# Kernel tuning notes

Hardware: AMD Instinct MI355X
Metric: run time of the kernel (lower is better)

## Reference

```python
import jax, jax.numpy as jnp
import numpy as np

H = W = 32          # gussin() is hard-coded to width=32 in BASE
C = 512             # BASE inner_nc; down conv is 1024->512
V = 1.5             # gaussian sigma


def _gaussian_weights():
    # Vectorized equivalent of gussin(1.5): g[p, x, y] for p = i*W + k,
    # g = exp(-((x-i)^2+(y-k)^2)/(2 v^2)) / (2 pi v^2), normalized per p.
    idx = np.arange(H, dtype=np.float64)
    d1 = (idx[:, None] - idx[None, :]) ** 2            # (i, x)
    d2 = d1[:, None, :, None] + d1[None, :, None, :]    # (i, k, x, y)
    g = np.exp(-d2 / (2.0 * V * V)) / (2.0 * np.pi * V * V)
    g = g.reshape(H * W, H, W)
    g = g / g.sum(axis=(1, 2), keepdims=True)
    return jnp.asarray(g, dtype=jnp.float32)


def _instance_norm(x, eps=1e-5):
    # InstanceNorm2d(affine=False): per-(b,c) mean/biased-var over (h,w)
    mu = x.mean(axis=(2, 3), keepdims=True)
    var = jnp.mean((x - mu) ** 2, axis=(2, 3), keepdims=True)
    return (x - mu) / jnp.sqrt(var + eps)


def _patches3(fm):
    # fm: (C, H+2, W+2) zero-padded map -> 3x3 patches: (H*W, C, 3, 3)
    p = jnp.stack([fm[:, di:di + H, dj:dj + W]
                   for di in range(3) for dj in range(3)], axis=-1)  # (C,H,W,9)
    return p.transpose(1, 2, 0, 3).reshape(H * W, C, 3, 3)


def setup_inputs() -> dict:
    key = jax.random.key(0)
    ks = jax.random.split(key, 4)
    x = jax.random.normal(ks[0], (1, C, H, W), jnp.float32)
    w_se1 = jax.random.normal(ks[1], (C // 16, C), jnp.float32) * 0.05   # SE squeeze fc
    w_se2 = jax.random.normal(ks[2], (C, C // 16), jnp.float32) * 0.05   # SE excite fc
    w_down = jax.random.normal(ks[3], (C, 2 * C, 1, 1), jnp.float32) * 0.05  # 1x1 conv 1024->512
    return {"x": x, "w_se1": w_se1, "w_se2": w_se2, "w_down": w_down}


def reference(x, w_se1, w_se2, w_down):
    gus = _gaussian_weights()                                # (HW, H, W), constant
    # --- SELayer(512, 16) ---
    s = x.mean(axis=(2, 3))                                  # (1, C) global avg pool
    s = jax.nn.relu(s @ w_se1.T)                             # (1, C/16)
    s = jax.nn.sigmoid(s @ w_se2.T)                          # (1, C)
    out32 = x * s[:, :, None, None]                          # (1, C, H, W)
    # --- gaussian-weighted pooling (einsum instead of (HW,C,H,W) broadcast) ---
    gus_out = jnp.einsum('pxy,cxy->pc', gus, out32[0])       # (HW, C)
    gus_out = gus_out.reshape(1, C, H, W)                    # raw reshape, as in torch .view
    # --- patch-based contextual self-attention (CSA) ---
    sig = jax.nn.sigmoid(out32)                              # (1, C, H, W)
    sig_pad = jnp.pad(sig[0], ((0, 0), (1, 1), (1, 1)))
    raw_pad = jnp.pad(out32[0], ((0, 0), (1, 1), (1, 1)))
    p_sig = _patches3(sig_pad)                               # (HW, C, 3, 3)
    p_raw = _patches3(raw_pad)                               # (HW, C, 3, 3)
    center = sig[0].transpose(1, 2, 0).reshape(H * W, C, 1, 1)  # center sigmoid vec per loc
    score = jnp.mean(center * p_sig, axis=1)                 # (HW, 3, 3)
    attn = jax.nn.softmax(score.reshape(H * W, 9), axis=1).reshape(H * W, 1, 3, 3)
    out_csa = jnp.sum(attn * p_raw, axis=(2, 3))             # (HW, C)
    out_csa = out_csa.reshape(1, C, H, W)                    # raw reshape, as in torch .view
    # --- concat + 1x1 conv down + InstanceNorm + LeakyReLU(0.2) ---
    cat = jnp.concatenate([gus_out, out_csa], axis=1)        # (1, 2C, H, W)
    y = jnp.einsum('bihw,oi->bohw', cat, w_down[:, :, 0, 0])
    y = _instance_norm(y)
    return jnp.where(y >= 0, y, 0.2 * y)
```

## Files before the change

### kernel.cpp

```cpp
#include <hip/hip_runtime.h>


typedef short short8 __attribute__((ext_vector_type(8)));
typedef short short4v __attribute__((ext_vector_type(4)));
typedef float floatx4 __attribute__((ext_vector_type(4)));

__device__ __forceinline__ unsigned short f2bf(float x) {
  union { float f; unsigned u; } v; v.f = x;
  unsigned u = v.u;
  u = (u + 0x7fffu + ((u >> 16) & 1u)) >> 16;
  return (unsigned short)u;
}

__device__ __forceinline__ float block_reduce_256(float v, float* sm4) {
  #pragma unroll
  for (int off = 32; off >= 1; off >>= 1) v += __shfl_down(v, off);
  __syncthreads();
  if ((threadIdx.x & 63) == 0) sm4[threadIdx.x >> 6] = v;
  __syncthreads();
  return sm4[0] + sm4[1] + sm4[2] + sm4[3];
}

__global__ void k_mean_gn(const float* __restrict__ x, float* __restrict__ smean,
                          float* __restrict__ gn, const float* __restrict__ wdn,
                          unsigned short* __restrict__ Abf) {
  if (blockIdx.x > 512) {
    int base = (blockIdx.x - 513) * 2048 + threadIdx.x * 8;
    float4 a = *(const float4*)&wdn[base];
    float4 b = *(const float4*)&wdn[base + 4];
    short8 s;
    s[0] = (short)f2bf(a.x); s[1] = (short)f2bf(a.y); s[2] = (short)f2bf(a.z); s[3] = (short)f2bf(a.w);
    s[4] = (short)f2bf(b.x); s[5] = (short)f2bf(b.y); s[6] = (short)f2bf(b.z); s[7] = (short)f2bf(b.w);
    *(short8*)&Abf[base] = s;
    return;
  }
  if (blockIdx.x == 512) {
    int tid = threadIdx.x;
    int a = tid >> 3;
    int b0 = (tid & 7) * 4;
    float e[4];
    float s = 0.0f;
    #pragma unroll
    for (int q = 0; q < 4; q++) {
      float d = (float)(a - (b0 + q));
      e[q] = __expf(d * d * (-1.0f / 4.5f));
      s += e[q];
    }
    s += __shfl_xor(s, 1, 8);
    s += __shfl_xor(s, 2, 8);
    s += __shfl_xor(s, 4, 8);
    float inv = 1.0f / s;
    #pragma unroll
    for (int q = 0; q < 4; q++) gn[a * 32 + b0 + q] = e[q] * inv;
    return;
  }
  __shared__ float sm4[4];
  int c = blockIdx.x;
  const float* row = x + c * 1024;
  float s = 0.0f;
  for (int i = threadIdx.x; i < 1024; i += 256) s += row[i];
  float t = block_reduce_256(s, sm4);
  if (threadIdx.x == 0) smean[c] = t * (1.0f / 1024.0f);
}

__global__ void k_apply(const float* __restrict__ x, const float* __restrict__ smean,
                        const float* __restrict__ w1, const float* __restrict__ w2,
                        float* __restrict__ out32T, float* __restrict__ sigT,
                        float* __restrict__ V) {
  __shared__ float sm[512];
  __shared__ float s1[32];
  __shared__ float sc[32];
  __shared__ float tile[32][33];
  int tid = threadIdx.x;
  for (int i = tid; i < 512; i += 256) sm[i] = smean[i];
  __syncthreads();
  int j = tid >> 3, l8 = tid & 7;
  float a = 0.0f;
  for (int cc = l8; cc < 512; cc += 8) a += sm[cc] * w1[j * 512 + cc];
  a += __shfl_down(a, 4, 8);
  a += __shfl_down(a, 2, 8);
  a += __shfl_down(a, 1, 8);
  if (l8 == 0) s1[j] = fmaxf(a, 0.0f);
  __syncthreads();
  int c0 = blockIdx.y * 32, hw0 = blockIdx.x * 32;
  if (tid < 32) {
    float b = 0.0f;
    #pragma unroll
    for (int jj = 0; jj < 32; jj++) b += s1[jj] * w2[(c0 + tid) * 32 + jj];
    sc[tid] = 1.0f / (1.0f + __expf(-b));
  }
  __syncthreads();
  int tx = tid & 31, ty = tid >> 5;
  #pragma unroll
  for (int r = 0; r < 4; r++) {
    int c = ty + 8 * r;
    float v = x[(c0 + c) * 1024 + hw0 + tx] * sc[c];
    tile[c][tx] = v;
  }
  __syncthreads();
  #pragma unroll
  for (int r = 0; r < 4; r++) {
    int hw = hw0 + ty + 8 * r;
    float v = tile[tx][ty + 8 * r];
    out32T[hw * 512 + c0 + tx] = v;
    sigT[hw * 512 + c0 + tx] = 1.0f / (1.0f + __expf(-v));
    int hwsw = ((hw & 31) << 5) | (hw >> 5);
    V[hwsw * 512 + c0 + tx] = v;
  }
}

__global__ void k_g1csa(const float* __restrict__ V, const float* __restrict__ gn,
                        const float* __restrict__ sigT, const float* __restrict__ out32T,
                        float* __restrict__ T1, unsigned short* __restrict__ catT) {
  if (blockIdx.x < 512) {
    __shared__ float g[1024];
    int tid = threadIdx.x;
    for (int i = tid; i < 1024; i += 256) g[i] = gn[i];
    __syncthreads();
    int t = blockIdx.x * 256 + tid;
    int c = t & 511;
    int xk = t >> 9;
    int xx = xk & 31, kg = xk >> 5;
    const float* vp = V + xx * 512 + c;
    const float* g0 = g + kg * 4 * 32;
    float s0 = 0, s1 = 0, s2 = 0, s3 = 0;
    #pragma unroll 8
    for (int y = 0; y < 32; y++) {
      float vv = vp[y * 16384];
      s0 += g0[y] * vv;
      s1 += g0[32 + y] * vv;
      s2 += g0[64 + y] * vv;
      s3 += g0[96 + y] * vv;
    }
    int ko = kg * 4 * 32 + xx;
    T1[ko * 512 + c] = s0;
    T1[(ko + 32) * 512 + c] = s1;
    T1[(ko + 64) * 512 + c] = s2;
    T1[(ko + 96) * 512 + c] = s3;
  } else {
    int wv = threadIdx.x >> 6;
    int lane = threadIdx.x & 63;
    int p = (blockIdx.x - 512) * 4 + wv;
    int h = p >> 5, w = p & 31;
    int c0 = lane * 8;
    float4 ce0 = *(const float4*)&sigT[p * 512 + c0];
    float4 ce1 = *(const float4*)&sigT[p * 512 + c0 + 4];
    int qoff[9];
    float s[9];
    #pragma unroll
    for (int dd = 0; dd < 9; dd++) {
      int hh = h + dd / 3 - 1, ww = w + (dd % 3) - 1;
      bool v = (hh >= 0) && (hh < 32) && (ww >= 0) && (ww < 32);
      qoff[dd] = v ? (hh * 32 + ww) * 512 : -1;
      float a = 0.0f;
      if (v) {
        float4 n0 = *(const float4*)&sigT[qoff[dd] + c0];
        float4 n1 = *(const float4*)&sigT[qoff[dd] + c0 + 4];
        a = ce0.x * n0.x + ce0.y * n0.y + ce0.z * n0.z + ce0.w * n0.w
          + ce1.x * n1.x + ce1.y * n1.y + ce1.z * n1.z + ce1.w * n1.w;
      }
      #pragma unroll
      for (int off = 32; off >= 1; off >>= 1) a += __shfl_xor(a, off);
      s[dd] = a;
    }
    float mx = -1e30f;
    #pragma unroll
    for (int dd = 0; dd < 9; dd++) { s[dd] *= (1.0f / 512.0f); mx = fmaxf(mx, s[dd]); }
    float tot = 0.0f;
    #pragma unroll
    for (int dd = 0; dd < 9; dd++) { s[dd] = __expf(s[dd] - mx); tot += s[dd]; }
    float inv = 1.0f / tot;
    float o[8] = {0, 0, 0, 0, 0, 0, 0, 0};
    #pragma unroll
    for (int dd = 0; dd < 9; dd++) {
      if (qoff[dd] >= 0) {
        float att = s[dd] * inv;
        float4 r0 = *(const float4*)&out32T[qoff[dd] + c0];
        float4 r1 = *(const float4*)&out32T[qoff[dd] + c0 + 4];
        o[0] += att * r0.x; o[1] += att * r0.y; o[2] += att * r0.z; o[3] += att * r0.w;
        o[4] += att * r1.x; o[5] += att * r1.y; o[6] += att * r1.z; o[7] += att * r1.w;
      }
    }
    int kcol = 512 + (p >> 1);
    int nbase = (p & 1) * 512 + c0;
    #pragma unroll
    for (int q = 0; q < 8; q++) catT[(nbase + q) * 1024 + kcol] = f2bf(o[q]);
  }
}

__global__ void k_g2(const float* __restrict__ T1, const float* __restrict__ gn,
                     unsigned short* __restrict__ catT) {
  __shared__ float g[1024];
  int tid = threadIdx.x;
  for (int i = tid; i < 1024; i += 256) g[i] = gn[i];
  __syncthreads();
  int t = blockIdx.x * 256 + tid;
  int c = t & 511;
  int rest = t >> 9;
  int i = rest >> 3;
  int sub = rest & 7;
  int par = sub & 1, kq = sub >> 1;
  const float* tp = T1 + c;
  const float* gi = g + i * 32;
  float s0 = 0, s1 = 0, s2 = 0, s3 = 0;
  int kb = kq * 8 + par;
  #pragma unroll 8
  for (int xx = 0; xx < 32; xx++) {
    float gv = gi[xx];
    s0 += gv * tp[((kb + 0) * 32 + xx) * 512];
    s1 += gv * tp[((kb + 2) * 32 + xx) * 512];
    s2 += gv * tp[((kb + 4) * 32 + xx) * 512];
    s3 += gv * tp[((kb + 6) * 32 + xx) * 512];
  }
  short4v o;
  o[0] = (short)f2bf(s0); o[1] = (short)f2bf(s1); o[2] = (short)f2bf(s2); o[3] = (short)f2bf(s3);
  *(short4v*)&catT[(par * 512 + c) * 1024 + i * 16 + kq * 4] = o;
}

__global__ void k_gemm(const unsigned short* __restrict__ Abf,
                       const unsigned short* __restrict__ Bbf,
                       float* __restrict__ yp) {
  int wv = threadIdx.x >> 6, lane = threadIdx.x & 63;
  int w0 = blockIdx.x;
  int m = w0 >> 4;
  int n0 = (w0 & 15) * 64;
  int nn = n0 + (wv & 1) * 32;
  int kz = wv >> 1;
  int l16 = lane & 15, quad = lane >> 4;
  const short8* ap  = (const short8*)(Abf + (m * 16 + l16) * 1024 + kz * 512 + quad * 8);
  const short8* bp0 = (const short8*)(Bbf + (nn + l16) * 1024 + kz * 512 + quad * 8);
  const short8* bp1 = (const short8*)(Bbf + (nn + 16 + l16) * 1024 + kz * 512 + quad * 8);
  floatx4 acc0 = {0.f, 0.f, 0.f, 0.f}, acc1 = {0.f, 0.f, 0.f, 0.f};
  #pragma unroll 4
  for (int kk = 0; kk < 16; kk++) {
    short8 a  = ap[kk * 4];
    short8 b0 = bp0[kk * 4];
    short8 b1 = bp1[kk * 4];
    acc0 = __builtin_amdgcn_mfma_f32_16x16x32_bf16(a, b0, acc0, 0, 0, 0);
    acc1 = __builtin_amdgcn_mfma_f32_16x16x32_bf16(a, b1, acc1, 0, 0, 0);
  }
  float* yo = yp + kz * 524288 + (m * 16 + quad * 4) * 1024 + l16;
  #pragma unroll
  for (int r = 0; r < 4; r++) {
    yo[r * 1024 + nn] = acc0[r];
    yo[r * 1024 + nn + 16] = acc1[r];
  }
}

__global__ void k_inorm(const float* __restrict__ yp, float* __restrict__ out) {
  __shared__ float sm4[4];
  __shared__ float vrow[1024];
  int o = blockIdx.x;
  const float* r0 = yp + o * 1024;
  float s = 0.0f, q = 0.0f;
  for (int i = threadIdx.x; i < 1024; i += 256) {
    float v = r0[i] + r0[i + 524288];
    vrow[i] = v;
    s += v; q += v * v;
  }
  float ts = block_reduce_256(s, sm4);
  float tq = block_reduce_256(q, sm4);
  float mean = ts * (1.0f / 1024.0f);
  float var = tq * (1.0f / 1024.0f) - mean * mean;
  float inv = rsqrtf(var + 1e-5f);
  for (int i = threadIdx.x; i < 1024; i += 256) {
    float v = (vrow[i] - mean) * inv;
    out[o * 1024 + i] = v >= 0.0f ? v : 0.2f * v;
  }
}

extern "C" void kernel_launch(void* const* d_in, const int* in_sizes, int n_in,
                              void* d_out, int out_size, void* d_ws, size_t ws_size,
                              hipStream_t stream) {
  const float* x      = (const float*)d_in[0];
  const float* w_se1  = (const float*)d_in[1];
  const float* w_se2  = (const float*)d_in[2];
  const float* w_down = (const float*)d_in[3];
  float* out = (float*)d_out;

  float* ws = (float*)d_ws;
  float* gn     = ws;
  float* smean  = ws + 1024;
  float* out32T = ws + 2048;
  float* sigT   = out32T + 524288;
  float* V      = sigT + 524288;
  float* T1     = V + 524288;
  unsigned short* catT = (unsigned short*)(T1 + 524288);
  unsigned short* Abf  = (unsigned short*)(T1 + 1048576);
  float* yp     = T1 + 1310720;

  k_mean_gn<<<769, 256, 0, stream>>>(x, smean, gn, w_down, Abf);
  k_apply<<<dim3(32, 16), 256, 0, stream>>>(x, smean, w_se1, w_se2, out32T, sigT, V);
  k_g1csa<<<768, 256, 0, stream>>>(V, gn, sigT, out32T, T1, catT);
  k_g2<<<512, 256, 0, stream>>>(T1, gn, catT);
  k_gemm<<<512, 256, 0, stream>>>(Abf, catT, yp);
  k_inorm<<<512, 256, 0, stream>>>(yp, out);
}
```

Measured before the change: 111.7 us.

## Fuse six kernels into one persistent kernel with atomic grid barriers

Replaces the six-kernel launch sequence with a single persistent kernel of 512 blocks. The stages are separated by software grid barriers built on atomic counters, which are reset by a memset before launch. The Gaussian table is now computed per block straight into shared memory instead of staged through global memory, and the CSA work is moved into two waves of the same blocks that run the first Gaussian pass. The aim is to remove launch gaps and inter-kernel drain; the cost is barrier spin overhead and a deadlock risk if not all 512 blocks are co-resident.

Result: slower. 357.9 us (+220.5%).

```diff
diff --git a/kernel.cpp b/kernel.cpp
--- a/kernel.cpp
+++ b/kernel.cpp
@@ -4,6 +4,8 @@
 typedef short short8 __attribute__((ext_vector_type(8)));
 typedef short short4v __attribute__((ext_vector_type(4)));
 typedef float floatx4 __attribute__((ext_vector_type(4)));
+
+#define NBLK 512
 
 __device__ __forceinline__ unsigned short f2bf(float x) {
   union { float f; unsigned u; } v; v.f = x;
@@ -21,251 +23,251 @@
   return sm4[0] + sm4[1] + sm4[2] + sm4[3];
 }
 
-__global__ void k_mean_gn(const float* __restrict__ x, float* __restrict__ smean,
-                          float* __restrict__ gn, const float* __restrict__ wdn,
-                          unsigned short* __restrict__ Abf) {
-  if (blockIdx.x > 512) {
-    int base = (blockIdx.x - 513) * 2048 + threadIdx.x * 8;
-    float4 a = *(const float4*)&wdn[base];
-    float4 b = *(const float4*)&wdn[base + 4];
-    short8 s;
-    s[0] = (short)f2bf(a.x); s[1] = (short)f2bf(a.y); s[2] = (short)f2bf(a.z); s[3] = (short)f2bf(a.w);
-    s[4] = (short)f2bf(b.x); s[5] = (short)f2bf(b.y); s[6] = (short)f2bf(b.z); s[7] = (short)f2bf(b.w);
-    *(short8*)&Abf[base] = s;
-    return;
-  }
-  if (blockIdx.x == 512) {
-    int tid = threadIdx.x;
-    int a = tid >> 3;
-    int b0 = (tid & 7) * 4;
-    float e[4];
-    float s = 0.0f;
-    #pragma unroll
-    for (int q = 0; q < 4; q++) {
-      float d = (float)(a - (b0 + q));
-      e[q] = __expf(d * d * (-1.0f / 4.5f));
-      s += e[q];
-    }
-    s += __shfl_xor(s, 1, 8);
-    s += __shfl_xor(s, 2, 8);
-    s += __shfl_xor(s, 4, 8);
-    float inv = 1.0f / s;
-    #pragma unroll
-    for (int q = 0; q < 4; q++) gn[a * 32 + b0 + q] = e[q] * inv;
-    return;
-  }
+__device__ __forceinline__ void gridbar(int* cnt, int ph) {
+  __syncthreads();
+  if (threadIdx.x == 0) {
+    __threadfence();
+    __hip_atomic_fetch_add(&cnt[ph], 1, __ATOMIC_RELAXED, __HIP_MEMORY_SCOPE_AGENT);
+    int it = 0;
+    while (__hip_atomic_load(&cnt[ph], __ATOMIC_RELAXED, __HIP_MEMORY_SCOPE_AGENT) < NBLK) {
+      __builtin_amdgcn_s_sleep(2);
+      if (++it > (1 << 24)) break;
+    }
+    __threadfence();
+  }
+  __syncthreads();
+}
+
+__global__ __launch_bounds__(256, 2) void k_fused(
+    const float* __restrict__ x, const float* __restrict__ w1,
+    const float* __restrict__ w2, const float* __restrict__ wdn,
+    int* __restrict__ cnt, float* __restrict__ smean,
+    float* __restrict__ out32T, float* __restrict__ sigT,
+    float* __restrict__ V, float* __restrict__ T1,
+    unsigned short* __restrict__ catT, unsigned short* __restrict__ Abf,
+    float* __restrict__ yp, float* __restrict__ out) {
   __shared__ float sm4[4];
-  int c = blockIdx.x;
-  const float* row = x + c * 1024;
-  float s = 0.0f;
-  for (int i = threadIdx.x; i < 1024; i += 256) s += row[i];
-  float t = block_reduce_256(s, sm4);
-  if (threadIdx.x == 0) smean[c] = t * (1.0f / 1024.0f);
-}
-
-__global__ void k_apply(const float* __restrict__ x, const float* __restrict__ smean,
-                        const float* __restrict__ w1, const float* __restrict__ w2,
-                        float* __restrict__ out32T, float* __restrict__ sigT,
-                        float* __restrict__ V) {
   __shared__ float sm[512];
   __shared__ float s1[32];
   __shared__ float sc[32];
   __shared__ float tile[32][33];
-  int tid = threadIdx.x;
-  for (int i = tid; i < 512; i += 256) sm[i] = smean[i];
-  __syncthreads();
-  int j = tid >> 3, l8 = tid & 7;
-  float a = 0.0f;
-  for (int cc = l8; cc < 512; cc += 8) a += sm[cc] * w1[j * 512 + cc];
-  a += __shfl_down(a, 4, 8);
-  a += __shfl_down(a, 2, 8);
-  a += __shfl_down(a, 1, 8);
-  if (l8 == 0) s1[j] = fmaxf(a, 0.0f);
-  __syncthreads();
-  int c0 = blockIdx.y * 32, hw0 = blockIdx.x * 32;
-  if (tid < 32) {
-    float b = 0.0f;
-    #pragma unroll
-    for (int jj = 0; jj < 32; jj++) b += s1[jj] * w2[(c0 + tid) * 32 + jj];
-    sc[tid] = 1.0f / (1.0f + __expf(-b));
-  }
-  __syncthreads();
-  int tx = tid & 31, ty = tid >> 5;
-  #pragma unroll
-  for (int r = 0; r < 4; r++) {
-    int c = ty + 8 * r;
-    float v = x[(c0 + c) * 1024 + hw0 + tx] * sc[c];
-    tile[c][tx] = v;
-  }
-  __syncthreads();
-  #pragma unroll
-  for (int r = 0; r < 4; r++) {
-    int hw = hw0 + ty + 8 * r;
-    float v = tile[tx][ty + 8 * r];
-    out32T[hw * 512 + c0 + tx] = v;
-    sigT[hw * 512 + c0 + tx] = 1.0f / (1.0f + __expf(-v));
-    int hwsw = ((hw & 31) << 5) | (hw >> 5);
-    V[hwsw * 512 + c0 + tx] = v;
-  }
-}
-
-__global__ void k_g1csa(const float* __restrict__ V, const float* __restrict__ gn,
-                        const float* __restrict__ sigT, const float* __restrict__ out32T,
-                        float* __restrict__ T1, unsigned short* __restrict__ catT) {
-  if (blockIdx.x < 512) {
-    __shared__ float g[1024];
-    int tid = threadIdx.x;
-    for (int i = tid; i < 1024; i += 256) g[i] = gn[i];
-    __syncthreads();
-    int t = blockIdx.x * 256 + tid;
+  __shared__ float g[1024];
+  __shared__ float vrow[1024];
+
+  const int tid = threadIdx.x;
+  const int b = blockIdx.x;
+
+  {
+    const float* row = x + b * 1024;
+    float s = 0.0f;
+    #pragma unroll
+    for (int i = tid; i < 1024; i += 256) s += row[i];
+    float t = block_reduce_256(s, sm4);
+    if (tid == 0) smean[b] = t * (1.0f / 1024.0f);
+    int base = b * 1024 + tid * 4;
+    float4 a4 = *(const float4*)&wdn[base];
+    short4v s4;
+    s4[0] = (short)f2bf(a4.x); s4[1] = (short)f2bf(a4.y);
+    s4[2] = (short)f2bf(a4.z); s4[3] = (short)f2bf(a4.w);
+    *(short4v*)&Abf[base] = s4;
+    int ga = tid >> 3, gb0 = (tid & 7) * 4;
+    float e[4]; float gs = 0.0f;
+    #pragma unroll
+    for (int q = 0; q < 4; q++) {
+      float d = (float)(ga - (gb0 + q));
+      e[q] = __expf(d * d * (-1.0f / 4.5f));
+      gs += e[q];
+    }
+    gs += __shfl_xor(gs, 1, 8);
+    gs += __shfl_xor(gs, 2, 8);
+    gs += __shfl_xor(gs, 4, 8);
+    float ginv = 1.0f / gs;
+    #pragma unroll
+    for (int q = 0; q < 4; q++) g[ga * 32 + gb0 + q] = e[q] * ginv;
+  }
+  gridbar(cnt, 0);
+
+  {
+    for (int i = tid; i < 512; i += 256) sm[i] = smean[i];
+    __syncthreads();
+    int j = tid >> 3, l8 = tid & 7;
+    float a = 0.0f;
+    for (int cc = l8; cc < 512; cc += 8) a += sm[cc] * w1[j * 512 + cc];
+    a += __shfl_down(a, 4, 8);
+    a += __shfl_down(a, 2, 8);
+    a += __shfl_down(a, 1, 8);
+    if (l8 == 0) s1[j] = fmaxf(a, 0.0f);
+    __syncthreads();
+    int c0 = (b & 15) * 32, hw0 = (b >> 4) * 32;
+    if (tid < 32) {
+      float bb = 0.0f;
+      #pragma unroll
+      for (int jj = 0; jj < 32; jj++) bb += s1[jj] * w2[(c0 + tid) * 32 + jj];
+      sc[tid] = 1.0f / (1.0f + __expf(-bb));
+    }
+    __syncthreads();
+    int tx = tid & 31, ty = tid >> 5;
+    #pragma unroll
+    for (int r = 0; r < 4; r++) {
+      int c = ty + 8 * r;
+      tile[c][tx] = x[(c0 + c) * 1024 + hw0 + tx] * sc[c];
+    }
+    __syncthreads();
+    #pragma unroll
+    for (int r = 0; r < 4; r++) {
+      int hw = hw0 + ty + 8 * r;
+      float v = tile[tx][ty + 8 * r];
+      out32T[hw * 512 + c0 + tx] = v;
+      sigT[hw * 512 + c0 + tx] = 1.0f / (1.0f + __expf(-v));
+      int hwsw = ((hw & 31) << 5) | (hw >> 5);
+      V[hwsw * 512 + c0 + tx] = v;
+    }
+  }
+  gridbar(cnt, 1);
+
+  {
+    int t = b * 256 + tid;
     int c = t & 511;
     int xk = t >> 9;
     int xx = xk & 31, kg = xk >> 5;
     const float* vp = V + xx * 512 + c;
-    const float* g0 = g + kg * 4 * 32;
-    float s0 = 0, s1 = 0, s2 = 0, s3 = 0;
+    const float* g0 = g + kg * 128;
+    float s0 = 0, s1v = 0, s2 = 0, s3 = 0;
     #pragma unroll 8
     for (int y = 0; y < 32; y++) {
       float vv = vp[y * 16384];
       s0 += g0[y] * vv;
-      s1 += g0[32 + y] * vv;
+      s1v += g0[32 + y] * vv;
       s2 += g0[64 + y] * vv;
       s3 += g0[96 + y] * vv;
     }
-    int ko = kg * 4 * 32 + xx;
+    int ko = kg * 128 + xx;
     T1[ko * 512 + c] = s0;
-    T1[(ko + 32) * 512 + c] = s1;
+    T1[(ko + 32) * 512 + c] = s1v;
     T1[(ko + 64) * 512 + c] = s2;
     T1[(ko + 96) * 512 + c] = s3;
-  } else {
-    int wv = threadIdx.x >> 6;
-    int lane = threadIdx.x & 63;
-    int p = (blockIdx.x - 512) * 4 + wv;
-    int h = p >> 5, w = p & 31;
-    int c0 = lane * 8;
-    float4 ce0 = *(const float4*)&sigT[p * 512 + c0];
-    float4 ce1 = *(const float4*)&sigT[p * 512 + c0 + 4];
-    int qoff[9];
-    float s[9];
-    #pragma unroll
-    for (int dd = 0; dd < 9; dd++) {
-      int hh = h + dd / 3 - 1, ww = w + (dd % 3) - 1;
-      bool v = (hh >= 0) && (hh < 32) && (ww >= 0) && (ww < 32);
-      qoff[dd] = v ? (hh * 32 + ww) * 512 : -1;
-      float a = 0.0f;
-      if (v) {
-        float4 n0 = *(const float4*)&sigT[qoff[dd] + c0];
-        float4 n1 = *(const float4*)&sigT[qoff[dd] + c0 + 4];
-        a = ce0.x * n0.x + ce0.y * n0.y + ce0.z * n0.z + ce0.w * n0.w
-          + ce1.x * n1.x + ce1.y * n1.y + ce1.z * n1.z + ce1.w * n1.w;
+
+    int wv = tid >> 6, lane = tid & 63;
+    if (wv < 2) {
+      int p = b * 2 + wv;
+      int h = p >> 5, w = p & 31;
+      int c0 = lane * 8;
+      float4 ce0 = *(const float4*)&sigT[p * 512 + c0];
+      float4 ce1 = *(const float4*)&sigT[p * 512 + c0 + 4];
+      int qoff[9];
+      float s[9];
+      #pragma unroll
+      for (int dd = 0; dd < 9; dd++) {
+        int hh = h + dd / 3 - 1, ww = w + (dd % 3) - 1;
+        bool v = (hh >= 0) && (hh < 32) && (ww >= 0) && (ww < 32);
+        qoff[dd] = v ? (hh * 32 + ww) * 512 : -1;
+        float a = 0.0f;
+        if (v) {
+          float4 n0 = *(const float4*)&sigT[qoff[dd] + c0];
+          float4 n1 = *(const float4*)&sigT[qoff[dd] + c0 + 4];
+          a = ce0.x * n0.x + ce0.y * n0.y + ce0.z * n0.z + ce0.w * n0.w
+            + ce1.x * n1.x + ce1.y * n1.y + ce1.z * n1.z + ce1.w * n1.w;
+        }
+        #pragma unroll
+        for (int off = 32; off >= 1; off >>= 1) a += __shfl_xor(a, off);
+        s[dd] = a;
       }
-      #pragma unroll
-      for (int off = 32; off >= 1; off >>= 1) a += __shfl_xor(a, off);
-      s[dd] = a;
-    }
-    float mx = -1e30f;
-    #pragma unroll
-    for (int dd = 0; dd < 9; dd++) { s[dd] *= (1.0f / 512.0f); mx = fmaxf(mx, s[dd]); }
-    float tot = 0.0f;
-    #pragma unroll
-    for (int dd = 0; dd < 9; dd++) { s[dd] = __expf(s[dd] - mx); tot += s[dd]; }
-    float inv = 1.0f / tot;
-    float o[8] = {0, 0, 0, 0, 0, 0, 0, 0};
-    #pragma unroll
-    for (int dd = 0; dd < 9; dd++) {
-      if (qoff[dd] >= 0) {
-        float att = s[dd] * inv;
-        float4 r0 = *(const float4*)&out32T[qoff[dd] + c0];
-        float4 r1 = *(const float4*)&out32T[qoff[dd] + c0 + 4];
-        o[0] += att * r0.x; o[1] += att * r0.y; o[2] += att * r0.z; o[3] += att * r0.w;
-        o[4] += att * r1.x; o[5] += att * r1.y; o[6] += att * r1.z; o[7] += att * r1.w;
+      float mx = -1e30f;
+      #pragma unroll
+      for (int dd = 0; dd < 9; dd++) { s[dd] *= (1.0f / 512.0f); mx = fmaxf(mx, s[dd]); }
+      float tot = 0.0f;
+      #pragma unroll
+      for (int dd = 0; dd < 9; dd++) { s[dd] = __expf(s[dd] - mx); tot += s[dd]; }
+      float inv = 1.0f / tot;
+      float o[8] = {0, 0, 0, 0, 0, 0, 0, 0};
+      #pragma unroll
+      for (int dd = 0; dd < 9; dd++) {
+        if (qoff[dd] >= 0) {
+          float att = s[dd] * inv;
+          float4 r0 = *(const float4*)&out32T[qoff[dd] + c0];
+          float4 r1 = *(const float4*)&out32T[qoff[dd] + c0 + 4];
+          o[0] += att * r0.x; o[1] += att * r0.y; o[2] += att * r0.z; o[3] += att * r0.w;
+          o[4] += att * r1.x; o[5] += att * r1.y; o[6] += att * r1.z; o[7] += att * r1.w;
+        }
       }
-    }
-    int kcol = 512 + (p >> 1);
-    int nbase = (p & 1) * 512 + c0;
-    #pragma unroll
-    for (int q = 0; q < 8; q++) catT[(nbase + q) * 1024 + kcol] = f2bf(o[q]);
-  }
-}
-
-__global__ void k_g2(const float* __restrict__ T1, const float* __restrict__ gn,
-                     unsigned short* __restrict__ catT) {
-  __shared__ float g[1024];
-  int tid = threadIdx.x;
-  for (int i = tid; i < 1024; i += 256) g[i] = gn[i];
-  __syncthreads();
-  int t = blockIdx.x * 256 + tid;
-  int c = t & 511;
-  int rest = t >> 9;
-  int i = rest >> 3;
-  int sub = rest & 7;
-  int par = sub & 1, kq = sub >> 1;
-  const float* tp = T1 + c;
-  const float* gi = g + i * 32;
-  float s0 = 0, s1 = 0, s2 = 0, s3 = 0;
-  int kb = kq * 8 + par;
-  #pragma unroll 8
-  for (int xx = 0; xx < 32; xx++) {
-    float gv = gi[xx];
-    s0 += gv * tp[((kb + 0) * 32 + xx) * 512];
-    s1 += gv * tp[((kb + 2) * 32 + xx) * 512];
-    s2 += gv * tp[((kb + 4) * 32 + xx) * 512];
-    s3 += gv * tp[((kb + 6) * 32 + xx) * 512];
-  }
-  short4v o;
-  o[0] = (short)f2bf(s0); o[1] = (short)f2bf(s1); o[2] = (short)f2bf(s2); o[3] = (short)f2bf(s3);
-  *(short4v*)&catT[(par * 512 + c) * 1024 + i * 16 + kq * 4] = o;
-}
-
-__global__ void k_gemm(const unsigned short* __restrict__ Abf,
-                       const unsigned short* __restrict__ Bbf,
-                       float* __restrict__ yp) {
-  int wv = threadIdx.x >> 6, lane = threadIdx.x & 63;
-  int w0 = blockIdx.x;
-  int m = w0 >> 4;
-  int n0 = (w0 & 15) * 64;
-  int nn = n0 + (wv & 1) * 32;
-  int kz = wv >> 1;
-  int l16 = lane & 15, quad = lane >> 4;
-  const short8* ap  = (const short8*)(Abf + (m * 16 + l16) * 1024 + kz * 512 + quad * 8);
-  const short8* bp0 = (const short8*)(Bbf + (nn + l16) * 1024 + kz * 512 + quad * 8);
-  const short8* bp1 = (const short8*)(Bbf + (nn + 16 + l16) * 1024 + kz * 512 + quad * 8);
-  floatx4 acc0 = {0.f, 0.f, 0.f, 0.f}, acc1 = {0.f, 0.f, 0.f, 0.f};
-  #pragma unroll 4
-  for (int kk = 0; kk < 16; kk++) {
-    short8 a  = ap[kk * 4];
-    short8 b0 = bp0[kk * 4];
-    short8 b1 = bp1[kk * 4];
-    acc0 = __builtin_amdgcn_mfma_f32_16x16x32_bf16(a, b0, acc0, 0, 0, 0);
-    acc1 = __builtin_amdgcn_mfma_f32_16x16x32_bf16(a, b1, acc1, 0, 0, 0);
-  }
-  float* yo = yp + kz * 524288 + (m * 16 + quad * 4) * 1024 + l16;
-  #pragma unroll
-  for (int r = 0; r < 4; r++) {
-    yo[r * 1024 + nn] = acc0[r];
-    yo[r * 1024 + nn + 16] = acc1[r];
-  }
-}
-
-__global__ void k_inorm(const float* __restrict__ yp, float* __restrict__ out) {
-  __shared__ float sm4[4];
-  __shared__ float vrow[1024];
-  int o = blockIdx.x;
-  const float* r0 = yp + o * 1024;
-  float s = 0.0f, q = 0.0f;
-  for (int i = threadIdx.x; i < 1024; i += 256) {
-    float v = r0[i] + r0[i + 524288];
-    vrow[i] = v;
-    s += v; q += v * v;
-  }
-  float ts = block_reduce_256(s, sm4);
-  float tq = block_reduce_256(q, sm4);
-  float mean = ts * (1.0f / 1024.0f);
-  float var = tq * (1.0f / 1024.0f) - mean * mean;
-  float inv = rsqrtf(var + 1e-5f);
-  for (int i = threadIdx.x; i < 1024; i += 256) {
-    float v = (vrow[i] - mean) * inv;
-    out[o * 1024 + i] = v >= 0.0f ? v : 0.2f * v;
+      int kcol = 512 + (p >> 1);
+      int nbase = (p & 1) * 512 + c0;
+      #pragma unroll
+      for (int q = 0; q < 8; q++) catT[(nbase + q) * 1024 + kcol] = f2bf(o[q]);
+    }
+  }
+  gridbar(cnt, 2);
+
+  {
+    int t = b * 256 + tid;
+    int c = t & 511;
+    int rest = t >> 9;
+    int i = rest >> 3;
+    int sub = rest & 7;
+    int par = sub & 1, kq = sub >> 1;
+    int kb = kq * 8 + par;
+    const float* tp = T1 + c;
+    const float* gi = g + i * 32;
+    float s0 = 0, s1v = 0, s2 = 0, s3 = 0;
+    #pragma unroll 8
+    for (int xx = 0; xx < 32; xx++) {
+      float gv = gi[xx];
+      s0 += gv * tp[((kb + 0) * 32 + xx) * 512];
+      s1v += gv * tp[((kb + 2) * 32 + xx) * 512];
+      s2 += gv * tp[((kb + 4) * 32 + xx) * 512];
+      s3 += gv * tp[((kb + 6) * 32 + xx) * 512];
+    }
+    short4v o;
+    o[0] = (short)f2bf(s0); o[1] = (short)f2bf(s1v);
+    o[2] = (short)f2bf(s2); o[3] = (short)f2bf(s3);
+    *(short4v*)&catT[(par * 512 + c) * 1024 + i * 16 + kq * 4] = o;
+  }
+  gridbar(cnt, 3);
+
+  {
+    int wv = tid >> 6, lane = tid & 63;
+    int m = b >> 4;
+    int nn = (b & 15) * 64 + (wv & 1) * 32;
+    int kz = wv >> 1;
+    int l16 = lane & 15, quad = lane >> 4;
+    const short8* ap  = (const short8*)(Abf + (m * 16 + l16) * 1024 + kz * 512 + quad * 8);
+    const short8* bp0 = (const short8*)(catT + (nn + l16) * 1024 + kz * 512 + quad * 8);
+    const short8* bp1 = (const short8*)(catT + (nn + 16 + l16) * 1024 + kz * 512 + quad * 8);
+    floatx4 acc0 = {0.f, 0.f, 0.f, 0.f}, acc1 = {0.f, 0.f, 0.f, 0.f};
+    #pragma unroll 4
+    for (int kk = 0; kk < 16; kk++) {
+      short8 a  = ap[kk * 4];
+      short8 b0 = bp0[kk * 4];
+      short8 b1 = bp1[kk * 4];
+      acc0 = __builtin_amdgcn_mfma_f32_16x16x32_bf16(a, b0, acc0, 0, 0, 0);
+      acc1 = __builtin_amdgcn_mfma_f32_16x16x32_bf16(a, b1, acc1, 0, 0, 0);
+    }
+    float* yo = yp + kz * 524288 + (m * 16 + quad * 4) * 1024 + l16;
+    #pragma unroll
+    for (int r = 0; r < 4; r++) {
+      yo[r * 1024 + nn] = acc0[r];
+      yo[r * 1024 + nn + 16] = acc1[r];
+    }
+  }
+  gridbar(cnt, 4);
+
+  {
+    const float* r0 = yp + b * 1024;
+    float s = 0.0f, q = 0.0f;
+    for (int i = tid; i < 1024; i += 256) {
+      float v = r0[i] + r0[i + 524288];
+      vrow[i] = v;
+      s += v; q += v * v;
+    }
+    float ts = block_reduce_256(s, sm4);
+    float tq = block_reduce_256(q, sm4);
+    float mean = ts * (1.0f / 1024.0f);
+    float var = tq * (1.0f / 1024.0f) - mean * mean;
+    float inv = rsqrtf(var + 1e-5f);
+    for (int i = tid; i < 1024; i += 256) {
+      float v = (vrow[i] - mean) * inv;
+      out[b * 1024 + i] = v >= 0.0f ? v : 0.2f * v;
+    }
   }
 }
 
@@ -279,20 +281,17 @@
   float* out = (float*)d_out;
 
   float* ws = (float*)d_ws;
-  float* gn     = ws;
+  int*   cnt    = (int*)ws;
   float* smean  = ws + 1024;
   float* out32T = ws + 2048;
-  float* sigT   = out32T + 524288;
-  float* V      = sigT + 524288;
-  float* T1     = V + 524288;
-  unsigned short* catT = (unsigned short*)(T1 + 524288);
-  unsigned short* Abf  = (unsigned short*)(T1 + 1048576);
-  float* yp     = T1 + 1310720;
-
-  k_mean_gn<<<769, 256, 0, stream>>>(x, smean, gn, w_down, Abf);
-  k_apply<<<dim3(32, 16), 256, 0, stream>>>(x, smean, w_se1, w_se2, out32T, sigT, V);
-  k_g1csa<<<768, 256, 0, stream>>>(V, gn, sigT, out32T, T1, catT);
-  k_g2<<<512, 256, 0, stream>>>(T1, gn, catT);
-  k_gemm<<<512, 256, 0, stream>>>(Abf, catT, yp);
-  k_inorm<<<512, 256, 0, stream>>>(yp, out);
-}
+  float* sigT   = ws + 526336;
+  float* V      = ws + 1050624;
+  float* T1     = ws + 1574912;
+  unsigned short* catT = (unsigned short*)(ws + 2099200);
+  unsigned short* Abf  = (unsigned short*)(ws + 2623488);
+  float* yp     = ws + 2885632;
+
+  hipMemsetAsync(cnt, 0, 64, stream);
+  k_fused<<<NBLK, 256, 0, stream>>>(x, w_se1, w_se2, w_down, cnt, smean,
+                                    out32T, sigT, V, T1, catT, Abf, yp, out);
+}
```

## Fuse separable gaussian passes per channel in LDS and use 32x32 MFMA GEMM

Applied to the files above, without the earlier changes.

The two separable gaussian-filter passes are merged into one block per channel that keeps the 32x32 map and the intermediate in shared memory. This removes the T1 global round trip, the swizzled V buffer and one kernel launch. Gaussian weights are now computed inside each block instead of by a separate block. The GEMM switches to 32x32x16 bf16 MFMA and reduces the split-K partial sums in LDS, so the instance-norm kernel no longer adds two partial buffers. The price is an extra plain-layout out32 write in k_apply and redundant per-block gaussian computation.

Result: faster. 102.8 us (-7.9%).

```diff
diff --git a/kernel.cpp b/kernel.cpp
--- a/kernel.cpp
+++ b/kernel.cpp
@@ -4,6 +4,7 @@
 typedef short short8 __attribute__((ext_vector_type(8)));
 typedef short short4v __attribute__((ext_vector_type(4)));
 typedef float floatx4 __attribute__((ext_vector_type(4)));
+typedef float floatx16 __attribute__((ext_vector_type(16)));
 
 __device__ __forceinline__ unsigned short f2bf(float x) {
   union { float f; unsigned u; } v; v.f = x;
@@ -21,11 +22,27 @@
   return sm4[0] + sm4[1] + sm4[2] + sm4[3];
 }
 
-__global__ void k_mean_gn(const float* __restrict__ x, float* __restrict__ smean,
-                          float* __restrict__ gn, const float* __restrict__ wdn,
-                          unsigned short* __restrict__ Abf) {
-  if (blockIdx.x > 512) {
-    int base = (blockIdx.x - 513) * 2048 + threadIdx.x * 8;
+__device__ __forceinline__ void gauss_lds(float* g, int tid) {
+  int ga = tid >> 3, gb0 = (tid & 7) * 4;
+  float e[4]; float gs = 0.0f;
+  #pragma unroll
+  for (int q = 0; q < 4; q++) {
+    float d = (float)(ga - (gb0 + q));
+    e[q] = __expf(d * d * (-1.0f / 4.5f));
+    gs += e[q];
+  }
+  gs += __shfl_xor(gs, 1, 8);
+  gs += __shfl_xor(gs, 2, 8);
+  gs += __shfl_xor(gs, 4, 8);
+  float ginv = 1.0f / gs;
+  #pragma unroll
+  for (int q = 0; q < 4; q++) g[ga * 32 + gb0 + q] = e[q] * ginv;
+}
+
+__global__ void k_mean_cvt(const float* __restrict__ x, float* __restrict__ smean,
+                           const float* __restrict__ wdn, unsigned short* __restrict__ Abf) {
+  if (blockIdx.x >= 512) {
+    int base = (blockIdx.x - 512) * 2048 + threadIdx.x * 8;
     float4 a = *(const float4*)&wdn[base];
     float4 b = *(const float4*)&wdn[base + 4];
     short8 s;
@@ -34,26 +51,6 @@
     *(short8*)&Abf[base] = s;
     return;
   }
-  if (blockIdx.x == 512) {
-    int tid = threadIdx.x;
-    int a = tid >> 3;
-    int b0 = (tid & 7) * 4;
-    float e[4];
-    float s = 0.0f;
-    #pragma unroll
-    for (int q = 0; q < 4; q++) {
-      float d = (float)(a - (b0 + q));
-      e[q] = __expf(d * d * (-1.0f / 4.5f));
-      s += e[q];
-    }
-    s += __shfl_xor(s, 1, 8);
-    s += __shfl_xor(s, 2, 8);
-    s += __shfl_xor(s, 4, 8);
-    float inv = 1.0f / s;
-    #pragma unroll
-    for (int q = 0; q < 4; q++) gn[a * 32 + b0 + q] = e[q] * inv;
-    return;
-  }
   __shared__ float sm4[4];
   int c = blockIdx.x;
   const float* row = x + c * 1024;
@@ -65,8 +62,8 @@
 
 __global__ void k_apply(const float* __restrict__ x, const float* __restrict__ smean,
                         const float* __restrict__ w1, const float* __restrict__ w2,
-                        float* __restrict__ out32T, float* __restrict__ sigT,
-                        float* __restrict__ V) {
+                        float* __restrict__ out32, float* __restrict__ out32T,
+                        float* __restrict__ sigT) {
   __shared__ float sm[512];
   __shared__ float s1[32];
   __shared__ float sc[32];
@@ -84,10 +81,10 @@
   __syncthreads();
   int c0 = blockIdx.y * 32, hw0 = blockIdx.x * 32;
   if (tid < 32) {
-    float b = 0.0f;
-    #pragma unroll
-    for (int jj = 0; jj < 32; jj++) b += s1[jj] * w2[(c0 + tid) * 32 + jj];
-    sc[tid] = 1.0f / (1.0f + __expf(-b));
+    float bb = 0.0f;
+    #pragma unroll
+    for (int jj = 0; jj < 32; jj++) bb += s1[jj] * w2[(c0 + tid) * 32 + jj];
+    sc[tid] = 1.0f / (1.0f + __expf(-bb));
   }
   __syncthreads();
   int tx = tid & 31, ty = tid >> 5;
@@ -95,6 +92,7 @@
   for (int r = 0; r < 4; r++) {
     int c = ty + 8 * r;
     float v = x[(c0 + c) * 1024 + hw0 + tx] * sc[c];
+    out32[(c0 + c) * 1024 + hw0 + tx] = v;
     tile[c][tx] = v;
   }
   __syncthreads();
@@ -104,39 +102,61 @@
     float v = tile[tx][ty + 8 * r];
     out32T[hw * 512 + c0 + tx] = v;
     sigT[hw * 512 + c0 + tx] = 1.0f / (1.0f + __expf(-v));
-    int hwsw = ((hw & 31) << 5) | (hw >> 5);
-    V[hwsw * 512 + c0 + tx] = v;
-  }
-}
-
-__global__ void k_g1csa(const float* __restrict__ V, const float* __restrict__ gn,
-                        const float* __restrict__ sigT, const float* __restrict__ out32T,
-                        float* __restrict__ T1, unsigned short* __restrict__ catT) {
+  }
+}
+
+__global__ void k_gausscsa(const float* __restrict__ out32, const float* __restrict__ sigT,
+                           const float* __restrict__ out32T, unsigned short* __restrict__ catT) {
   if (blockIdx.x < 512) {
     __shared__ float g[1024];
+    __shared__ float row[32 * 33];
+    __shared__ float T[32 * 33];
+    int c = blockIdx.x;
     int tid = threadIdx.x;
-    for (int i = tid; i < 1024; i += 256) g[i] = gn[i];
+    gauss_lds(g, tid);
+    for (int idx = tid; idx < 1024; idx += 256)
+      row[(idx >> 5) * 33 + (idx & 31)] = out32[c * 1024 + idx];
     __syncthreads();
-    int t = blockIdx.x * 256 + tid;
-    int c = t & 511;
-    int xk = t >> 9;
-    int xx = xk & 31, kg = xk >> 5;
-    const float* vp = V + xx * 512 + c;
-    const float* g0 = g + kg * 4 * 32;
-    float s0 = 0, s1 = 0, s2 = 0, s3 = 0;
-    #pragma unroll 8
-    for (int y = 0; y < 32; y++) {
-      float vv = vp[y * 16384];
-      s0 += g0[y] * vv;
-      s1 += g0[32 + y] * vv;
-      s2 += g0[64 + y] * vv;
-      s3 += g0[96 + y] * vv;
-    }
-    int ko = kg * 4 * 32 + xx;
-    T1[ko * 512 + c] = s0;
-    T1[(ko + 32) * 512 + c] = s1;
-    T1[(ko + 64) * 512 + c] = s2;
-    T1[(ko + 96) * 512 + c] = s3;
+    {
+      int xx = tid & 31, kg = tid >> 5;
+      const float* g0 = g + kg * 128;
+      const float* rw = row + xx * 33;
+      float s0 = 0, s1 = 0, s2 = 0, s3 = 0;
+      #pragma unroll 8
+      for (int y = 0; y < 32; y++) {
+        float vv = rw[y];
+        s0 += g0[y] * vv;
+        s1 += g0[32 + y] * vv;
+        s2 += g0[64 + y] * vv;
+        s3 += g0[96 + y] * vv;
+      }
+      int k0 = kg * 4;
+      T[(k0 + 0) * 33 + xx] = s0;
+      T[(k0 + 1) * 33 + xx] = s1;
+      T[(k0 + 2) * 33 + xx] = s2;
+      T[(k0 + 3) * 33 + xx] = s3;
+    }
+    __syncthreads();
+    {
+      int i = tid >> 3;
+      int sub = tid & 7;
+      int par = sub & 1, kq = sub >> 1;
+      int kb = kq * 8 + par;
+      const float* gi = g + i * 32;
+      float s0 = 0, s1 = 0, s2 = 0, s3 = 0;
+      #pragma unroll 8
+      for (int xx = 0; xx < 32; xx++) {
+        float gv = gi[xx];
+        s0 += gv * T[(kb + 0) * 33 + xx];
+        s1 += gv * T[(kb + 2) * 33 + xx];
+        s2 += gv * T[(kb + 4) * 33 + xx];
+        s3 += gv * T[(kb + 6) * 33 + xx];
+      }
+      short4v o;
+      o[0] = (short)f2bf(s0); o[1] = (short)f2bf(s1);
+      o[2] = (short)f2bf(s2); o[3] = (short)f2bf(s3);
+      *(short4v*)&catT[(par * 512 + c) * 1024 + i * 16 + kq * 4] = o;
+    }
   } else {
     int wv = threadIdx.x >> 6;
     int lane = threadIdx.x & 63;
@@ -188,73 +208,48 @@
   }
 }
 
-__global__ void k_g2(const float* __restrict__ T1, const float* __restrict__ gn,
-                     unsigned short* __restrict__ catT) {
-  __shared__ float g[1024];
-  int tid = threadIdx.x;
-  for (int i = tid; i < 1024; i += 256) g[i] = gn[i];
-  __syncthreads();
-  int t = blockIdx.x * 256 + tid;
-  int c = t & 511;
-  int rest = t >> 9;
-  int i = rest >> 3;
-  int sub = rest & 7;
-  int par = sub & 1, kq = sub >> 1;
-  const float* tp = T1 + c;
-  const float* gi = g + i * 32;
-  float s0 = 0, s1 = 0, s2 = 0, s3 = 0;
-  int kb = kq * 8 + par;
-  #pragma unroll 8
-  for (int xx = 0; xx < 32; xx++) {
-    float gv = gi[xx];
-    s0 += gv * tp[((kb + 0) * 32 + xx) * 512];
-    s1 += gv * tp[((kb + 2) * 32 + xx) * 512];
-    s2 += gv * tp[((kb + 4) * 32 + xx) * 512];
-    s3 += gv * tp[((kb + 6) * 32 + xx) * 512];
-  }
-  short4v o;
-  o[0] = (short)f2bf(s0); o[1] = (short)f2bf(s1); o[2] = (short)f2bf(s2); o[3] = (short)f2bf(s3);
-  *(short4v*)&catT[(par * 512 + c) * 1024 + i * 16 + kq * 4] = o;
-}
-
 __global__ void k_gemm(const unsigned short* __restrict__ Abf,
                        const unsigned short* __restrict__ Bbf,
-                       float* __restrict__ yp) {
-  int wv = threadIdx.x >> 6, lane = threadIdx.x & 63;
-  int w0 = blockIdx.x;
-  int m = w0 >> 4;
-  int n0 = (w0 & 15) * 64;
-  int nn = n0 + (wv & 1) * 32;
-  int kz = wv >> 1;
-  int l16 = lane & 15, quad = lane >> 4;
-  const short8* ap  = (const short8*)(Abf + (m * 16 + l16) * 1024 + kz * 512 + quad * 8);
-  const short8* bp0 = (const short8*)(Bbf + (nn + l16) * 1024 + kz * 512 + quad * 8);
-  const short8* bp1 = (const short8*)(Bbf + (nn + 16 + l16) * 1024 + kz * 512 + quad * 8);
-  floatx4 acc0 = {0.f, 0.f, 0.f, 0.f}, acc1 = {0.f, 0.f, 0.f, 0.f};
-  #pragma unroll 4
-  for (int kk = 0; kk < 16; kk++) {
-    short8 a  = ap[kk * 4];
-    short8 b0 = bp0[kk * 4];
-    short8 b1 = bp1[kk * 4];
-    acc0 = __builtin_amdgcn_mfma_f32_16x16x32_bf16(a, b0, acc0, 0, 0, 0);
-    acc1 = __builtin_amdgcn_mfma_f32_16x16x32_bf16(a, b1, acc1, 0, 0, 0);
-  }
-  float* yo = yp + kz * 524288 + (m * 16 + quad * 4) * 1024 + l16;
-  #pragma unroll
-  for (int r = 0; r < 4; r++) {
-    yo[r * 1024 + nn] = acc0[r];
-    yo[r * 1024 + nn + 16] = acc1[r];
-  }
-}
-
-__global__ void k_inorm(const float* __restrict__ yp, float* __restrict__ out) {
+                       float* __restrict__ y) {
+  __shared__ float red[2][1024];
+  int tid = threadIdx.x;
+  int wv = tid >> 6, lane = tid & 63;
+  int nt = wv & 1, kz = wv >> 1;
+  int bm = (blockIdx.x >> 4) * 32;
+  int nn = (blockIdx.x & 15) * 64 + nt * 32;
+  int l32 = lane & 31, half = lane >> 5;
+  const short8* ap = (const short8*)(Abf + (bm + l32) * 1024 + kz * 512 + half * 8);
+  const short8* bp = (const short8*)(Bbf + (nn + l32) * 1024 + kz * 512 + half * 8);
+  floatx16 acc = {};
+  #pragma unroll 8
+  for (int ks = 0; ks < 32; ks++) {
+    short8 a = ap[ks * 2];
+    short8 b = bp[ks * 2];
+    acc = __builtin_amdgcn_mfma_f32_32x32x16_bf16(a, b, acc, 0, 0, 0);
+  }
+  if (kz == 1) {
+    #pragma unroll
+    for (int r = 0; r < 16; r++) red[nt][lane * 16 + r] = acc[r];
+  }
+  __syncthreads();
+  if (kz == 0) {
+    #pragma unroll
+    for (int r = 0; r < 16; r++) {
+      float v = acc[r] + red[nt][lane * 16 + r];
+      int rowm = (r & 3) + 8 * (r >> 2) + 4 * half;
+      y[(bm + rowm) * 1024 + nn + l32] = v;
+    }
+  }
+}
+
+__global__ void k_inorm(const float* __restrict__ y, float* __restrict__ out) {
   __shared__ float sm4[4];
   __shared__ float vrow[1024];
   int o = blockIdx.x;
-  const float* r0 = yp + o * 1024;
+  const float* r0 = y + o * 1024;
   float s = 0.0f, q = 0.0f;
   for (int i = threadIdx.x; i < 1024; i += 256) {
-    float v = r0[i] + r0[i + 524288];
+    float v = r0[i];
     vrow[i] = v;
     s += v; q += v * v;
   }
@@ -279,20 +274,17 @@
   float* out = (float*)d_out;
 
   float* ws = (float*)d_ws;
-  float* gn     = ws;
-  float* smean  = ws + 1024;
-  float* out32T = ws + 2048;
-  float* sigT   = out32T + 524288;
-  float* V      = sigT + 524288;
-  float* T1     = V + 524288;
-  unsigned short* catT = (unsigned short*)(T1 + 524288);
-  unsigned short* Abf  = (unsigned short*)(T1 + 1048576);
-  float* yp     = T1 + 1310720;
-
-  k_mean_gn<<<769, 256, 0, stream>>>(x, smean, gn, w_down, Abf);
-  k_apply<<<dim3(32, 16), 256, 0, stream>>>(x, smean, w_se1, w_se2, out32T, sigT, V);
-  k_g1csa<<<768, 256, 0, stream>>>(V, gn, sigT, out32T, T1, catT);
-  k_g2<<<512, 256, 0, stream>>>(T1, gn, catT);
-  k_gemm<<<512, 256, 0, stream>>>(Abf, catT, yp);
-  k_inorm<<<512, 256, 0, stream>>>(yp, out);
-}
+  float* smean  = ws;
+  float* out32  = ws + 1024;
+  float* out32T = ws + 525312;
+  float* sigT   = ws + 1049600;
+  unsigned short* catT = (unsigned short*)(ws + 1573888);
+  unsigned short* Abf  = (unsigned short*)(ws + 2098176);
+  float* ybuf   = ws + 2360320;
+
+  k_mean_cvt<<<768, 256, 0, stream>>>(x, smean, w_down, Abf);
+  k_apply<<<dim3(32, 16), 256, 0, stream>>>(x, smean, w_se1, w_se2, out32, out32T, sigT);
+  k_gausscsa<<<768, 256, 0, stream>>>(out32, sigT, out32T, catT);
+  k_gemm<<<256, 256, 0, stream>>>(Abf, catT, ybuf);
+  k_inorm<<<512, 256, 0, stream>>>(ybuf, out);
+}
```
